# Optimization experiments

Measured on AMD Instinct MI355X. Metric: run time of the kernel, lower is better.

## Reference

```python
import jax, jax.numpy as jnp
import numpy as np

RES = 0.03
NUM_ROTS = 36
NUM_PROPOSAL = 256
OVERSAMPLE = 4           # fixed-size stand-in for the data-dependent while loop
GX, GY, GZ = 272, 112, 272  # grid covering [-4,4.16] x [-0.2,3.16] x [-4,4.16] at res=0.03
POW = 0.5
SEED_DIST_THRESH = 0.3


def setup_inputs() -> dict:
    key = jax.random.key(0)
    ks = jax.random.split(key, 6)
    N, M = 100000, 1024
    extent = jnp.array([7.0, 3.0, 7.0], jnp.float32)
    offset = jnp.array([-3.5, 0.0, -3.5], jnp.float32)
    pc = jax.random.uniform(ks[0], (N, 3), jnp.float32) * extent + offset
    xyz = jax.random.uniform(ks[1], (N, 3), jnp.float32, minval=-0.3, maxval=0.3)
    scale = jax.random.uniform(ks[2], (N, 3), jnp.float32, minval=0.1, maxval=1.0)
    prob = jax.random.uniform(ks[3], (N,), jnp.float32)
    corners = jnp.array([[-4.0, -0.2, -4.0], [4.16, 3.16, 4.16]], jnp.float32)
    vote_points = jax.random.uniform(ks[4], (M, 3), jnp.float32) * extent + offset
    return dict(pc=pc, xyz=xyz, scale=scale, prob=prob, corners=corners, vote_points=vote_points)


def hough_vote(pc, xyz, scale, prob, corners):
    # Each point casts NUM_ROTS votes: center = pc + R_y(theta) @ xyz_offset
    thetas = 2.0 * jnp.pi * jnp.arange(NUM_ROTS, dtype=jnp.float32) / NUM_ROTS
    c, s = jnp.cos(thetas), jnp.sin(thetas)  # [R]
    ox, oy, oz = xyz[:, 0:1], xyz[:, 1:2], xyz[:, 2:3]  # [N,1]
    rx = ox * c + oz * s      # [N,R]
    rz = -ox * s + oz * c     # [N,R]
    tx = pc[:, 0:1] + rx
    ty = jnp.broadcast_to(pc[:, 1:2] + oy, tx.shape)
    tz = pc[:, 2:3] + rz
    ix = jnp.floor((tx - corners[0, 0]) / RES + 0.5).astype(jnp.int32)
    iy = jnp.floor((ty - corners[0, 1]) / RES + 0.5).astype(jnp.int32)
    iz = jnp.floor((tz - corners[0, 2]) / RES + 0.5).astype(jnp.int32)
    inb = ((ix >= 0) & (ix < GX) & (iy >= 0) & (iy < GY) & (iz >= 0) & (iz < GZ))
    ixc = jnp.clip(ix, 0, GX - 1)
    iyc = jnp.clip(iy, 0, GY - 1)
    izc = jnp.clip(iz, 0, GZ - 1)
    flat = ((ixc * GY + iyc) * GZ + izc).ravel()  # [N*R]
    w = (prob[:, None] * inb.astype(prob.dtype))  # [N,R]
    grid_obj = jnp.zeros((GX * GY * GZ,), pc.dtype).at[flat].add(w.ravel())
    ws = (w[:, :, None] * scale[:, None, :]).reshape(-1, 3)
    grid_scale = jnp.zeros((GX * GY * GZ, 3), pc.dtype).at[flat].add(ws)
    hv_map = grid_obj.reshape(GX, GY, GZ)
    hv_scale = (grid_scale / (grid_obj[:, None] + 1e-7)).reshape(GX, GY, GZ, 3)
    return hv_map, hv_scale


def reference(pc, xyz, scale, prob, corners, vote_points):
    hv_map, hv_scale = hough_vote(pc, xyz, scale, prob, corners)
    hv_map_y = jnp.power(hv_map.max(axis=1) + 1e-7, POW)  # [GX,GZ]
    hv_map_yidx = jnp.argmax(hv_map, axis=1)              # [GX,GZ]
    dist = hv_map_y.reshape(-1)
    finite = jnp.isfinite(dist)
    safe = jnp.where(finite, dist, 0.0)
    ok = finite.all() & (safe.sum() >= 1e-7)
    dist = jnp.where(ok, safe, 1.0)

    # fixed-size oversampling instead of the data-dependent while loop
    K = NUM_PROPOSAL * OVERSAMPLE
    sample = jax.random.categorical(jax.random.key(42), jnp.log(dist + 1e-30), shape=(K,))
    sample_val = dist[sample]
    xi = sample // GZ
    zi = sample % GZ
    yi = hv_map_yidx[xi, zi]
    world_loc = jnp.stack([xi, yi, zi], -1).astype(pc.dtype) * RES + corners[0]  # [K,3]
    sc = hv_scale[xi, yi, zi, :]  # [K,3]

    # min distance to vote seeds; keep candidates near seeds (fallback: keep all)
    d2seed = jnp.min(jnp.linalg.norm(world_loc[:, None, :] - vote_points[None, :, :], axis=-1), axis=-1)
    keep = d2seed < SEED_DIST_THRESH
    keep = jnp.where(keep.any(), keep, jnp.ones_like(keep))
    order = jnp.argsort(jnp.where(keep, 0, 1))  # stable: passing candidates first
    sel = order[:NUM_PROPOSAL]
    candidates = world_loc[sel]
    scales_out = sc[sel]
    probs = jnp.zeros((NUM_PROPOSAL,), pc.dtype)
    return candidates, probs, scales_out
```

## Files before the change

### kernel.cpp

```cpp
#include <hip/hip_runtime.h>
#include <math.h>
#include <stdio.h>
#include <stdint.h>

#define GXD 272
#define GYD 112
#define GZD 272
#define NROT 36
#define CCLS (GXD*GZD)
#define CBLK (CCLS/256)
#define KSMP 1024
#define NPROP 256
#define HSLOTS 2048
#define YH 56
#define NBINS (GXD*2)
#define SLICE (GYD*GZD)
#define SVCAP 96
#define AROWS 32
#define AUNITS (CBLK * (KSMP/AROWS))
#define TH_SPEC 0xFFE00000u

struct RotTab { float c[NROT]; float s[NROT]; };

__device__ __forceinline__ uint32_t cell_hash(int flat) {
    return ((uint32_t)flat * 2654435761u) >> 21;
}

#define ROTL_AB(x, r) __builtin_amdgcn_alignbit((x), (x), 32u - (r))

__device__ __forceinline__ uint32_t tf_bits(uint32_t i) {
    constexpr uint32_t K1  = 42u;
    constexpr uint32_t KS2 = 42u ^ 0x1BD11BDAu;
    uint32_t x0 = 0u, x1 = i + K1;
#define TF_R(r)  { x0 += x1; x1 = ROTL_AB(x1, r); x1 ^= x0; }
#define TF_RI(r, I0, I1) { x1 += (I1); x0 = x0 + (I0) + x1; x1 = ROTL_AB(x1, r); x1 ^= x0; }
    TF_R(13) TF_R(15) TF_R(26) TF_R(6)
    TF_RI(17, K1,  KS2 + 1u)  TF_R(29) TF_R(16) TF_R(24)
    TF_RI(13, KS2, 2u)        TF_R(15) TF_R(26) TF_R(6)
    TF_RI(17, 0u,  K1 + 3u)   TF_R(29) TF_R(16) TF_R(24)
    TF_RI(13, K1,  KS2 + 4u)  TF_R(15) TF_R(26) TF_R(6)
#undef TF_R
#undef TF_RI
    return (x0 + KS2) ^ (x1 + 5u);
}

__device__ __forceinline__ float uniform_from_bits(uint32_t b) {
    const float TINY = 1.1754943508222875e-38f;
    float f = __uint_as_float((b >> 9) | 0x3f800000u) - 1.0f;
    float u = __fadd_rn(__fmul_rn(f, 1.0f), TINY);
    return fmaxf(TINY, u);
}

__device__ __forceinline__ float gumbel_from_u(float u) {
    float l1 = (float)log((double)u);
    float l2 = (float)log((double)(-l1));
    return -l2;
}

__device__ __forceinline__ void phaseA_unit(int unit, int* __restrict__ svcnt,
                                            uint2* __restrict__ svrec) {
    int cb = unit % CBLK;
    int rg = unit / CBLK;
    int c  = cb * 256 + threadIdx.x;
    int k0 = rg * AROWS;
    uint32_t i = (uint32_t)k0 * (uint32_t)CCLS + (uint32_t)c;
#pragma unroll 4
    for (int kk = 0; kk < AROWS; ++kk) {
        uint32_t bits = tf_bits(i);
        if (__builtin_expect(bits >= TH_SPEC, 0)) {
            int row = k0 + kk;
            int idx = atomicAdd(&svcnt[row], 1);
            if (idx < SVCAP) svrec[row * SVCAP + idx] = make_uint2((uint32_t)c, bits);
        }
        i += (uint32_t)CCLS;
    }
}

__device__ __forceinline__ bool vote_iy(float py, float oy, float c0y, int& iy) {
    float ty = __fadd_rn(py, oy);
    float vy = __fadd_rn(__fdiv_rn(__fsub_rn(ty, c0y), 0.03f), 0.5f);
    iy = (int)floorf(vy);
    return (iy >= 0 && iy < GYD);
}
__device__ __forceinline__ bool vote_xz(float px, float pz, float ox, float oz,
                                        float c, float s, float c0x, float c0z,
                                        int& ix, int& iz) {
    float rx = __fadd_rn(__fmul_rn(ox, c), __fmul_rn(oz, s));
    float rz = __fadd_rn(__fmul_rn(-ox, s), __fmul_rn(oz, c));
    float tx = __fadd_rn(px, rx);
    float tz = __fadd_rn(pz, rz);
    float vx = __fadd_rn(__fdiv_rn(__fsub_rn(tx, c0x), 0.03f), 0.5f);
    float vz = __fadd_rn(__fdiv_rn(__fsub_rn(tz, c0z), 0.03f), 0.5f);
    ix = (int)floorf(vx);
    iz = (int)floorf(vz);
    return (ix >= 0 && ix < GXD && iz >= 0 && iz < GZD);
}

__global__ __launch_bounds__(256) void k_count_b(const float* __restrict__ pc, const float* __restrict__ xyz,
                          const float* __restrict__ corners, int N, RotTab rt,
                          int* __restrict__ bincnt, int* __restrict__ hblk,
                          int nOrig, int unitBase, int* __restrict__ svcnt, uint2* __restrict__ svrec) {
    if ((int)blockIdx.x >= nOrig) { phaseA_unit(unitBase + (int)blockIdx.x - nOrig, svcnt, svrec); return; }
    __shared__ int h[NBINS];
    int tid = threadIdx.x;
    for (int j = tid; j < NBINS; j += 256) h[j] = 0;
    __syncthreads();
    int i = blockIdx.x * 256 + tid;
    if (i < N) {
        float px = pc[3*i], py = pc[3*i+1], pz = pc[3*i+2];
        float ox = xyz[3*i], oy = xyz[3*i+1], oz = xyz[3*i+2];
        int iy;
        if (vote_iy(py, oy, corners[1], iy)) {
            int ybit = (iy >= YH) ? 1 : 0;
            float c0x = corners[0], c0z = corners[2];
            for (int r = 0; r < NROT; ++r) {
                int ix, iz;
                if (vote_xz(px, pz, ox, oz, rt.c[r], rt.s[r], c0x, c0z, ix, iz))
                    atomicAdd(&h[ix*2 + ybit], 1);
            }
        }
    }
    __syncthreads();
    int* hb = hblk + (size_t)blockIdx.x * NBINS;
    for (int j = tid; j < NBINS; j += 256) {
        int cnt = h[j];
        hb[j] = cnt;
        if (cnt) atomicAdd(&bincnt[j], cnt);
    }
}

__global__ __launch_bounds__(576) void k_prefix(const int* __restrict__ bincnt,
                         int* __restrict__ binbase, int* __restrict__ bincur) {
    __shared__ int sc[576];
    int tid = threadIdx.x;
    int v = (tid < NBINS) ? bincnt[tid] : 0;
    sc[tid] = v;
    __syncthreads();
    for (int off = 1; off < 576; off <<= 1) {
        int x = sc[tid];
        if (tid >= off) x += sc[tid - off];
        __syncthreads();
        sc[tid] = x;
        __syncthreads();
    }
    if (tid < NBINS) {
        int excl = sc[tid] - v;
        binbase[tid] = excl;
        bincur[tid] = excl;
    }
}

__global__ __launch_bounds__(256) void k_binwrite_b(const float* __restrict__ pc, const float* __restrict__ xyz,
                          const float* __restrict__ corners,
                          int N, RotTab rt, int* __restrict__ bincur,
                          const int* __restrict__ hblk, uint32_t* __restrict__ vrec,
                          int nOrig, int unitBase, int* __restrict__ svcnt, uint2* __restrict__ svrec) {
    if ((int)blockIdx.x >= nOrig) { phaseA_unit(unitBase + (int)blockIdx.x - nOrig, svcnt, svrec); return; }
    __shared__ int h[NBINS];
    __shared__ int bbase[NBINS];
    int tid = threadIdx.x;
    const int* hb = hblk + (size_t)blockIdx.x * NBINS;
    for (int j = tid; j < NBINS; j += 256) {
        int cnt = hb[j];
        bbase[j] = cnt ? atomicAdd(&bincur[j], cnt) : 0;
        h[j] = 0;
    }
    __syncthreads();
    int i = blockIdx.x * 256 + tid;
    if (i < N) {
        float px = pc[3*i], py = pc[3*i+1], pz = pc[3*i+2];
        float ox = xyz[3*i], oy = xyz[3*i+1], oz = xyz[3*i+2];
        int iy;
        if (vote_iy(py, oy, corners[1], iy)) {
            int ybit = (iy >= YH) ? 1 : 0;
            int iyrel = iy - ybit*YH;
            float c0x = corners[0], c0z = corners[2];
            for (int r = 0; r < NROT; ++r) {
                int ix, iz;
                if (vote_xz(px, pz, ox, oz, rt.c[r], rt.s[r], c0x, c0z, ix, iz)) {
                    int bin = ix*2 + ybit;
                    int rank = atomicAdd(&h[bin], 1);
                    int slot = bbase[bin] + rank;
                    vrec[slot] = ((uint32_t)i << 14) | (uint32_t)(iyrel*GZD + iz);
                }
            }
        }
    }
}

__global__ __launch_bounds__(256) void k_accum(const int* __restrict__ binbase,
                          const int* __restrict__ bincnt,
                          const uint32_t* __restrict__ vrec,
                          const float* __restrict__ prob,
                          unsigned long long* __restrict__ packed) {
    __shared__ float tile[YH*GZD];
    int b = blockIdx.x;
    int x = b >> 1, yh = b & 1;
    int tid = threadIdx.x;
    for (int j = tid; j < YH*GZD; j += 256) tile[j] = 0.0f;
    __syncthreads();
    int lo = binbase[b], n = bincnt[b];
    for (int j = lo + tid; j < lo + n; j += 256) {
        uint32_t rec = vrec[j];
        atomicAdd(&tile[rec & 0x3FFFu], prob[rec >> 14]);
    }
    __syncthreads();
    int ybase = yh * YH;
    for (int z = tid; z < GZD; z += 256) {
        float m = tile[z];
        int mi = 0;
        for (int y = 1; y < YH; ++y) {
            float v = tile[y*GZD + z];
            if (v > m) { m = v; mi = y; }
        }
        unsigned long long key = ((unsigned long long)__float_as_uint(m) << 32)
                               | (unsigned long long)(uint32_t)(0x7F - (ybase + mi));
        atomicMax(&packed[x*GZD + z], key);
    }
}

__global__ __launch_bounds__(256) void k_colmax2_b(const unsigned long long* __restrict__ packed,
                         float* __restrict__ logits, int* __restrict__ yidx,
                         float* __restrict__ sumdist,
                         int nOrig, int unitBase, int* __restrict__ svcnt, uint2* __restrict__ svrec) {
    if ((int)blockIdx.x >= nOrig) { phaseA_unit(unitBase + (int)blockIdx.x - nOrig, svcnt, svrec); return; }
    int c = blockIdx.x * 256 + threadIdx.x;
    unsigned long long key = packed[c];
    float m = __uint_as_float((uint32_t)(key >> 32));
    int mi = 0x7F - (int)(uint32_t)(key & 0xFFFFFFFFu);
    float d = __fsqrt_rn(__fadd_rn(m, 1e-7f));
    yidx[c] = mi;
    logits[c] = (float)log((double)__fadd_rn(d, 1e-30f));
    __shared__ float sred[256];
    int tid = threadIdx.x;
    sred[tid] = d; __syncthreads();
    for (int off = 128; off > 0; off >>= 1) {
        if (tid < off) sred[tid] += sred[tid+off];
        __syncthreads();
    }
    if (tid == 0) atomicAdd(sumdist, sred[0]);
}

__global__ __launch_bounds__(256) void k_hotthresh_b(const float* __restrict__ logits,
                                                     const float* __restrict__ sumdist,
                                                     uint32_t* __restrict__ bth,
                                                     int* __restrict__ hotcnt, int* __restrict__ hotlist,
                                                     int nOrig, int unitBase,
                                                     int* __restrict__ svcnt, uint2* __restrict__ svrec) {
    if ((int)blockIdx.x >= nOrig) { phaseA_unit(unitBase + (int)blockIdx.x - nOrig, svcnt, svrec); return; }
    int c = blockIdx.x * 256 + threadIdx.x;
    double B0 = log((double)*sumdist) - 3.0;
    double t = exp(-exp((double)logits[c] - (B0 - 0.05)));
    long long k_th = (long long)floor(t * 8388608.0) - 2;
    uint32_t b;
    if (k_th <= 0)              b = 0u;
    else if (k_th >= 8388608LL) b = 0xFFFFFFFFu;
    else                        b = (uint32_t)k_th << 9;
    bth[c] = b;
    if (b < TH_SPEC) {
        int idx = atomicAdd(hotcnt, 1);
        hotlist[idx] = c;
    }
}

__global__ __launch_bounds__(256) void k_phaseB(const uint32_t* __restrict__ bth,
                                                const int* __restrict__ hotlist,
                                                const int* __restrict__ hotcnt,
                                                int* __restrict__ svcnt, uint2* __restrict__ svrec) {
    int k = blockIdx.x;
    int n = *hotcnt;
    uint32_t base = (uint32_t)k * (uint32_t)CCLS;
    for (int j = threadIdx.x; j < n; j += 256) {
        int c = hotlist[j];
        uint32_t bits = tf_bits(base + (uint32_t)c);
        if (bits >= bth[c] && bits < TH_SPEC) {
            int idx = atomicAdd(&svcnt[k], 1);
            if (idx < SVCAP) svrec[k * SVCAP + idx] = make_uint2((uint32_t)c, bits);
        }
    }
}

__global__ __launch_bounds__(64) void k_finalize(const float* __restrict__ logits,
                                                 const float* __restrict__ sumdist,
                                                 const int* __restrict__ svcnt,
                                                 const uint2* __restrict__ svrec,
                                                 const int* __restrict__ yidx,
                                                 int* __restrict__ hkeys,
                                                 int* __restrict__ samples) {
    int k = blockIdx.x;
    int tid = threadIdx.x;
    int n = svcnt[k];
    float best = -INFINITY; int bc = 0x7fffffff;
    bool full = (n <= 0 || n > SVCAP);
    if (!full) {
        for (int j = tid; j < n; j += 64) {
            uint2 rec = svrec[k * SVCAP + j];
            int c = (int)rec.x;
            float v = __fadd_rn(gumbel_from_u(uniform_from_bits(rec.y)), logits[c]);
            if (v > best || (v == best && c < bc)) { best = v; bc = c; }
        }
        for (int off = 32; off > 0; off >>= 1) {
            float v2 = __shfl_xor(best, off);
            int   i2 = __shfl_xor(bc, off);
            if (v2 > best || (v2 == best && i2 < bc)) { best = v2; bc = i2; }
        }
        double B0 = log((double)*sumdist) - 3.0;
        if (!((double)best > B0 - 0.05)) full = true;
    }
    if (full) {
        best = -INFINITY; bc = 0x7fffffff;
        uint32_t base = (uint32_t)k * (uint32_t)CCLS;
        for (int c = tid; c < CCLS; c += 64) {
            float v = __fadd_rn(gumbel_from_u(uniform_from_bits(tf_bits(base + (uint32_t)c))), logits[c]);
            if (v > best || (v == best && c < bc)) { best = v; bc = c; }
        }
        for (int off = 32; off > 0; off >>= 1) {
            float v2 = __shfl_xor(best, off);
            int   i2 = __shfl_xor(bc, off);
            if (v2 > best || (v2 == best && i2 < bc)) { best = v2; bc = i2; }
        }
    }
    if (tid == 0) {
        samples[k] = bc;
        int xi = bc / GZD, zi = bc % GZD;
        int yi = yidx[bc];
        int flat = (xi*GYD + yi)*GZD + zi;
        uint32_t h = cell_hash(flat);
        for (;;) {
            int prev = atomicCAS(&hkeys[h], -1, flat);
            if (prev == -1 || prev == flat) break;
            h = (h + 1) & (HSLOTS - 1);
        }
    }
}

__global__ __launch_bounds__(256) void k_scale_scatter(const float* __restrict__ pc, const float* __restrict__ xyz,
                          const float* __restrict__ scale, const float* __restrict__ prob,
                          const float* __restrict__ corners,
                          const int* __restrict__ hkeys, float* __restrict__ gsmall,
                          int N, RotTab rt) {
    __shared__ int lk[HSLOTS];
    for (int j = threadIdx.x; j < HSLOTS; j += 256) lk[j] = hkeys[j];
    __syncthreads();
    int i = blockIdx.x * 256 + threadIdx.x;
    if (i >= N) return;
    float px = pc[3*i], py = pc[3*i+1], pz = pc[3*i+2];
    float ox = xyz[3*i], oy = xyz[3*i+1], oz = xyz[3*i+2];
    int iy;
    if (!vote_iy(py, oy, corners[1], iy)) return;
    float c0x = corners[0], c0z = corners[2];
    int iyo = iy * GZD;
    float w0 = prob[i];
    float ws0 = __fmul_rn(w0, scale[3*i]);
    float ws1 = __fmul_rn(w0, scale[3*i+1]);
    float ws2 = __fmul_rn(w0, scale[3*i+2]);
    for (int r = 0; r < NROT; ++r) {
        int ix, iz;
        if (!vote_xz(px, pz, ox, oz, rt.c[r], rt.s[r], c0x, c0z, ix, iz)) continue;
        int flat = ix * SLICE + iyo + iz;
        uint32_t h = cell_hash(flat);
        int slot = -1;
        for (;;) {
            int key = lk[h];
            if (key == flat) { slot = (int)h; break; }
            if (key == -1) break;
            h = (h + 1) & (HSLOTS - 1);
        }
        if (slot < 0) continue;
        atomicAdd(&gsmall[3*slot+0], ws0);
        atomicAdd(&gsmall[3*slot+1], ws1);
        atomicAdd(&gsmall[3*slot+2], ws2);
    }
}

__global__ __launch_bounds__(256) void k_post(const unsigned long long* __restrict__ packed,
                       const int* __restrict__ hkeys, const float* __restrict__ gsmall,
                       const int* __restrict__ yidx, const int* __restrict__ samples,
                       const float* __restrict__ corners, const float* __restrict__ vp, int M,
                       float* __restrict__ world, float* __restrict__ scv, int* __restrict__ keep) {
    int k = blockIdx.x;
    int tid = threadIdx.x;
    int s = samples[k];
    int xi = s / GZD, zi = s % GZD;
    int yi = yidx[s];
    float wx = __fadd_rn(__fmul_rn((float)xi, 0.03f), corners[0]);
    float wy = __fadd_rn(__fmul_rn((float)yi, 0.03f), corners[1]);
    float wz = __fadd_rn(__fmul_rn((float)zi, 0.03f), corners[2]);

    float dmin = INFINITY;
    for (int j = tid; j < M; j += 256) {
        float dx = __fsub_rn(wx, vp[3*j]);
        float dy = __fsub_rn(wy, vp[3*j+1]);
        float dz = __fsub_rn(wz, vp[3*j+2]);
        float sq = __fadd_rn(__fadd_rn(__fmul_rn(dx,dx), __fmul_rn(dy,dy)), __fmul_rn(dz,dz));
        dmin = fminf(dmin, __fsqrt_rn(sq));
    }
    __shared__ float sm[256];
    sm[tid] = dmin; __syncthreads();
    for (int off = 128; off > 0; off >>= 1) {
        if (tid < off) sm[tid] = fminf(sm[tid], sm[tid+off]);
        __syncthreads();
    }
    if (tid == 0) {
        world[3*k] = wx; world[3*k+1] = wy; world[3*k+2] = wz;
        int flat = (xi*GYD + yi)*GZD + zi;
        uint32_t h = cell_hash(flat);
        while (hkeys[h] != flat) h = (h + 1) & (HSLOTS - 1);
        float m = __uint_as_float((uint32_t)(packed[s] >> 32));
        float go = __fadd_rn(m, 1e-7f);
        scv[3*k+0] = __fdiv_rn(gsmall[3*h+0], go);
        scv[3*k+1] = __fdiv_rn(gsmall[3*h+1], go);
        scv[3*k+2] = __fdiv_rn(gsmall[3*h+2], go);
        keep[k] = (sm[0] < 0.3f) ? 1 : 0;
    }
}

__global__ __launch_bounds__(256) void k_select(const float* __restrict__ world,
                                                const float* __restrict__ scv,
                                                const int* __restrict__ keep,
                                                float* __restrict__ out) {
    __shared__ int kp[KSMP];
    __shared__ int tsum[256];
    __shared__ int sel[NPROP];
    __shared__ int anyk;
    int tid = threadIdx.x;
    if (tid == 0) anyk = 0;
    __syncthreads();
    int a = 0;
    for (int j = tid; j < KSMP; j += 256) { int v = keep[j]; kp[j] = v; a |= v; }
    if (a) anyk = 1;
    __syncthreads();
    int any = anyk;
    int j0 = tid * 4;
    int k0v = any ? kp[j0]   : 1;
    int k1v = any ? kp[j0+1] : 1;
    int k2v = any ? kp[j0+2] : 1;
    int k3v = any ? kp[j0+3] : 1;
    int s0 = k0v, s1 = s0 + k1v, s2 = s1 + k2v, s3 = s2 + k3v;
    tsum[tid] = s3;
    __syncthreads();
    for (int off = 1; off < 256; off <<= 1) {
        int x = tsum[tid];
        if (tid >= off) x += tsum[tid - off];
        __syncthreads();
        tsum[tid] = x;
        __syncthreads();
    }
    int base = (tid > 0) ? tsum[tid-1] : 0;
    int nk = tsum[255];
    int inc[4] = { base + s0, base + s1, base + s2, base + s3 };
    int kv[4]  = { k0v, k1v, k2v, k3v };
    for (int q = 0; q < 4; ++q) {
        int j = j0 + q;
        int slot = kv[q] ? (inc[q] - 1) : (nk + j - inc[q]);
        if (slot < NPROP) sel[slot] = j;
    }
    __syncthreads();
    if (tid < NPROP) {
        int sidx = sel[tid];
        out[3*tid+0] = world[3*sidx+0];
        out[3*tid+1] = world[3*sidx+1];
        out[3*tid+2] = world[3*sidx+2];
        out[3*NPROP + tid] = 0.0f;
        out[4*NPROP + 3*tid + 0] = scv[3*sidx+0];
        out[4*NPROP + 3*tid + 1] = scv[3*sidx+1];
        out[4*NPROP + 3*tid + 2] = scv[3*sidx+2];
    }
}

extern "C" void kernel_launch(void* const* d_in, const int* in_sizes, int n_in,
                              void* d_out, int out_size, void* d_ws, size_t ws_size,
                              hipStream_t stream) {
    const float* pc      = (const float*)d_in[0];
    const float* xyz     = (const float*)d_in[1];
    const float* scale   = (const float*)d_in[2];
    const float* prob    = (const float*)d_in[3];
    const float* corners = (const float*)d_in[4];
    const float* vp      = (const float*)d_in[5];
    int N = in_sizes[0] / 3;
    int M = in_sizes[5] / 3;
    int NV = N * NROT;
    int pblocks = (N + 255) / 256;
    if (N > (1 << 17)) {
        fprintf(stderr, "kernel_launch: N %d exceeds packing limit\n", N);
        return;
    }

    float* sumdist = (float*)d_ws;
    int*   bincnt  = (int*)(sumdist + 1);
    int*   svcnt   = bincnt + NBINS;
    int*   hotcnt  = svcnt + KSMP;
    unsigned long long* packed = (unsigned long long*)(hotcnt + 1);
    float* gsmall  = (float*)(packed + CCLS);
    size_t zero_bytes = (size_t)((char*)(gsmall + 3*HSLOTS) - (char*)sumdist);
    int*   binbase = (int*)(gsmall + 3*HSLOTS);
    int*   bincur  = binbase + NBINS;
    float* logits  = (float*)(bincur + NBINS);
    uint32_t* bth  = (uint32_t*)(logits + CCLS);
    int*   yidx    = (int*)(bth + CCLS);
    int*   samples = yidx + CCLS;
    int*   hkeys   = samples + KSMP;
    float* world   = (float*)(hkeys + HSLOTS);
    float* scv     = world + 3*KSMP;
    int*   keep    = (int*)(scv + 3*KSMP);
    uint2* svrec   = (uint2*)(((uintptr_t)(keep + KSMP) + 15) & ~(uintptr_t)15);
    int*   hotlist = (int*)(svrec + (size_t)KSMP * SVCAP);
    int*   hblk    = hotlist + CCLS;
    uint32_t* vrec = (uint32_t*)(((uintptr_t)(hblk + (size_t)pblocks*NBINS) + 15) & ~(uintptr_t)15);
    size_t need = (size_t)((char*)(vrec + NV) - (char*)d_ws);
    if (ws_size < need) {
        fprintf(stderr, "kernel_launch: ws_size %zu < needed %zu\n", ws_size, need);
        return;
    }

    hipMemsetAsync(sumdist, 0, zero_bytes, stream);
    hipMemsetAsync(hkeys, 0xFF, HSLOTS*sizeof(int), stream);

    RotTab rt;
    const float twopi = (float)(2.0 * M_PI);
    for (int r = 0; r < NROT; ++r) {
        float th = (twopi * (float)r) / 36.0f;
        rt.c[r] = (float)cos((double)th);
        rt.s[r] = (float)sin((double)th);
    }

    const int BAL1 = 2800, BAL2 = 2800, BAL3 = 1900, BAL4 = AUNITS - BAL1 - BAL2 - BAL3;

    k_count_b<<<pblocks + BAL1, 256, 0, stream>>>(pc, xyz, corners, N, rt, bincnt, hblk,
                                                  pblocks, 0, svcnt, svrec);
    k_prefix<<<1, 576, 0, stream>>>(bincnt, binbase, bincur);
    k_binwrite_b<<<pblocks + BAL2, 256, 0, stream>>>(pc, xyz, corners, N, rt, bincur, hblk, vrec,
                                                     pblocks, BAL1, svcnt, svrec);
    k_accum<<<NBINS, 256, 0, stream>>>(binbase, bincnt, vrec, prob, packed);
    k_colmax2_b<<<CBLK + BAL3, 256, 0, stream>>>(packed, logits, yidx, sumdist,
                                                 CBLK, BAL1 + BAL2, svcnt, svrec);
    k_hotthresh_b<<<CBLK + BAL4, 256, 0, stream>>>(logits, sumdist, bth, hotcnt, hotlist,
                                                   CBLK, BAL1 + BAL2 + BAL3, svcnt, svrec);
    k_phaseB<<<KSMP, 256, 0, stream>>>(bth, hotlist, hotcnt, svcnt, svrec);
    k_finalize<<<KSMP, 64, 0, stream>>>(logits, sumdist, svcnt, svrec, yidx, hkeys, samples);
    k_scale_scatter<<<pblocks, 256, 0, stream>>>(pc, xyz, scale, prob, corners, hkeys, gsmall, N, rt);
    k_post<<<KSMP, 256, 0, stream>>>(packed, hkeys, gsmall, yidx, samples, corners, vp, M, world, scv, keep);
    k_select<<<1, 256, 0, stream>>>(world, scv, keep, (float*)d_out);
}
```

Measured before the change: 368.6 us.

## Cache vote bins across passes, fuse phaseB into finalize, bin-driven scale scatter

The count pass now stores each point-rotation's bin and cell code in a vote cache, so the binwrite pass reads these codes back instead of recomputing rotations and floor divisions. The phaseB kernel is folded into finalize, which scans the hot list itself with 64 threads per sample. The scale scatter now walks the binned vote records instead of recomputing votes per point, and it absorbs the last share of phaseA work units. The hash keys are shifted by one so that zero marks an empty slot, which lets a single memset clear them and drops one memset. In exchange the vote cache adds a large workspace write and read, and finalize has fewer threads for the hot-list scan.

```diff
diff --git a/kernel.cpp b/kernel.cpp
--- a/kernel.cpp
+++ b/kernel.cpp
@@ -19,6 +19,7 @@
 #define AROWS 32
 #define AUNITS (CBLK * (KSMP/AROWS))
 #define TH_SPEC 0xFFE00000u
+#define VC_INVALID 0xFFFFFFFFu
 
 struct RotTab { float c[NROT]; float s[NROT]; };
 
@@ -99,6 +100,7 @@
 __global__ __launch_bounds__(256) void k_count_b(const float* __restrict__ pc, const float* __restrict__ xyz,
                           const float* __restrict__ corners, int N, RotTab rt,
                           int* __restrict__ bincnt, int* __restrict__ hblk,
+                          uint32_t* __restrict__ vcache,
                           int nOrig, int unitBase, int* __restrict__ svcnt, uint2* __restrict__ svrec) {
     if ((int)blockIdx.x >= nOrig) { phaseA_unit(unitBase + (int)blockIdx.x - nOrig, svcnt, svrec); return; }
     __shared__ int h[NBINS];
@@ -106,19 +108,32 @@
     for (int j = tid; j < NBINS; j += 256) h[j] = 0;
     __syncthreads();
     int i = blockIdx.x * 256 + tid;
+    bool act = false;
+    float px=0, py=0, pz=0, ox=0, oy=0, oz=0, c0x=0, c0z=0;
+    int ybit = 0, iyrel = 0;
     if (i < N) {
-        float px = pc[3*i], py = pc[3*i+1], pz = pc[3*i+2];
-        float ox = xyz[3*i], oy = xyz[3*i+1], oz = xyz[3*i+2];
+        px = pc[3*i]; py = pc[3*i+1]; pz = pc[3*i+2];
+        ox = xyz[3*i]; oy = xyz[3*i+1]; oz = xyz[3*i+2];
         int iy;
         if (vote_iy(py, oy, corners[1], iy)) {
-            int ybit = (iy >= YH) ? 1 : 0;
-            float c0x = corners[0], c0z = corners[2];
-            for (int r = 0; r < NROT; ++r) {
-                int ix, iz;
-                if (vote_xz(px, pz, ox, oz, rt.c[r], rt.s[r], c0x, c0z, ix, iz))
-                    atomicAdd(&h[ix*2 + ybit], 1);
+            act = true;
+            ybit = (iy >= YH) ? 1 : 0;
+            iyrel = iy - ybit*YH;
+            c0x = corners[0]; c0z = corners[2];
+        }
+    }
+    uint32_t* vc = vcache + ((size_t)blockIdx.x * NROT) * 256 + tid;
+    for (int r = 0; r < NROT; ++r) {
+        uint32_t v = VC_INVALID;
+        if (act) {
+            int ix, iz;
+            if (vote_xz(px, pz, ox, oz, rt.c[r], rt.s[r], c0x, c0z, ix, iz)) {
+                int bin = ix*2 + ybit;
+                v = ((uint32_t)bin << 14) | (uint32_t)(iyrel*GZD + iz);
+                atomicAdd(&h[bin], 1);
             }
         }
+        vc[(size_t)r * 256] = v;
     }
     __syncthreads();
     int* hb = hblk + (size_t)blockIdx.x * NBINS;
@@ -150,10 +165,9 @@
     }
 }
 
-__global__ __launch_bounds__(256) void k_binwrite_b(const float* __restrict__ pc, const float* __restrict__ xyz,
-                          const float* __restrict__ corners,
-                          int N, RotTab rt, int* __restrict__ bincur,
-                          const int* __restrict__ hblk, uint32_t* __restrict__ vrec,
+__global__ __launch_bounds__(256) void k_binwrite_b(int N, int* __restrict__ bincur,
+                          const int* __restrict__ hblk, const uint32_t* __restrict__ vcache,
+                          uint32_t* __restrict__ vrec,
                           int nOrig, int unitBase, int* __restrict__ svcnt, uint2* __restrict__ svrec) {
     if ((int)blockIdx.x >= nOrig) { phaseA_unit(unitBase + (int)blockIdx.x - nOrig, svcnt, svrec); return; }
     __shared__ int h[NBINS];
@@ -166,24 +180,15 @@
         h[j] = 0;
     }
     __syncthreads();
-    int i = blockIdx.x * 256 + tid;
-    if (i < N) {
-        float px = pc[3*i], py = pc[3*i+1], pz = pc[3*i+2];
-        float ox = xyz[3*i], oy = xyz[3*i+1], oz = xyz[3*i+2];
-        int iy;
-        if (vote_iy(py, oy, corners[1], iy)) {
-            int ybit = (iy >= YH) ? 1 : 0;
-            int iyrel = iy - ybit*YH;
-            float c0x = corners[0], c0z = corners[2];
-            for (int r = 0; r < NROT; ++r) {
-                int ix, iz;
-                if (vote_xz(px, pz, ox, oz, rt.c[r], rt.s[r], c0x, c0z, ix, iz)) {
-                    int bin = ix*2 + ybit;
-                    int rank = atomicAdd(&h[bin], 1);
-                    int slot = bbase[bin] + rank;
-                    vrec[slot] = ((uint32_t)i << 14) | (uint32_t)(iyrel*GZD + iz);
-                }
-            }
+    uint32_t i = (uint32_t)(blockIdx.x * 256 + tid);
+    const uint32_t* vc = vcache + ((size_t)blockIdx.x * NROT) * 256 + tid;
+    uint32_t ish = i << 14;
+    for (int r = 0; r < NROT; ++r) {
+        uint32_t v = vc[(size_t)r * 256];
+        if (v != VC_INVALID) {
+            int bin = (int)(v >> 14);
+            int rank = atomicAdd(&h[bin], 1);
+            vrec[bbase[bin] + rank] = ish | (v & 0x3FFFu);
         }
     }
 }
@@ -263,33 +268,20 @@
     }
 }
 
-__global__ __launch_bounds__(256) void k_phaseB(const uint32_t* __restrict__ bth,
-                                                const int* __restrict__ hotlist,
-                                                const int* __restrict__ hotcnt,
-                                                int* __restrict__ svcnt, uint2* __restrict__ svrec) {
-    int k = blockIdx.x;
-    int n = *hotcnt;
-    uint32_t base = (uint32_t)k * (uint32_t)CCLS;
-    for (int j = threadIdx.x; j < n; j += 256) {
-        int c = hotlist[j];
-        uint32_t bits = tf_bits(base + (uint32_t)c);
-        if (bits >= bth[c] && bits < TH_SPEC) {
-            int idx = atomicAdd(&svcnt[k], 1);
-            if (idx < SVCAP) svrec[k * SVCAP + idx] = make_uint2((uint32_t)c, bits);
-        }
-    }
-}
-
 __global__ __launch_bounds__(64) void k_finalize(const float* __restrict__ logits,
                                                  const float* __restrict__ sumdist,
                                                  const int* __restrict__ svcnt,
                                                  const uint2* __restrict__ svrec,
+                                                 const uint32_t* __restrict__ bth,
+                                                 const int* __restrict__ hotlist,
+                                                 const int* __restrict__ hotcnt,
                                                  const int* __restrict__ yidx,
                                                  int* __restrict__ hkeys,
                                                  int* __restrict__ samples) {
     int k = blockIdx.x;
     int tid = threadIdx.x;
     int n = svcnt[k];
+    uint32_t base = (uint32_t)k * (uint32_t)CCLS;
     float best = -INFINITY; int bc = 0x7fffffff;
     bool full = (n <= 0 || n > SVCAP);
     if (!full) {
@@ -299,6 +291,15 @@
             float v = __fadd_rn(gumbel_from_u(uniform_from_bits(rec.y)), logits[c]);
             if (v > best || (v == best && c < bc)) { best = v; bc = c; }
         }
+        int nhot = *hotcnt;
+        for (int j = tid; j < nhot; j += 64) {
+            int c = hotlist[j];
+            uint32_t bits = tf_bits(base + (uint32_t)c);
+            if (bits >= bth[c] && bits < TH_SPEC) {
+                float v = __fadd_rn(gumbel_from_u(uniform_from_bits(bits)), logits[c]);
+                if (v > best || (v == best && c < bc)) { best = v; bc = c; }
+            }
+        }
         for (int off = 32; off > 0; off >>= 1) {
             float v2 = __shfl_xor(best, off);
             int   i2 = __shfl_xor(bc, off);
@@ -309,7 +310,6 @@
     }
     if (full) {
         best = -INFINITY; bc = 0x7fffffff;
-        uint32_t base = (uint32_t)k * (uint32_t)CCLS;
         for (int c = tid; c < CCLS; c += 64) {
             float v = __fadd_rn(gumbel_from_u(uniform_from_bits(tf_bits(base + (uint32_t)c))), logits[c]);
             if (v > best || (v == best && c < bc)) { best = v; bc = c; }
@@ -324,52 +324,47 @@
         samples[k] = bc;
         int xi = bc / GZD, zi = bc % GZD;
         int yi = yidx[bc];
-        int flat = (xi*GYD + yi)*GZD + zi;
-        uint32_t h = cell_hash(flat);
+        int key = (xi*GYD + yi)*GZD + zi + 1;
+        uint32_t h = cell_hash(key - 1);
         for (;;) {
-            int prev = atomicCAS(&hkeys[h], -1, flat);
-            if (prev == -1 || prev == flat) break;
+            int prev = atomicCAS(&hkeys[h], 0, key);
+            if (prev == 0 || prev == key) break;
             h = (h + 1) & (HSLOTS - 1);
         }
     }
 }
 
-__global__ __launch_bounds__(256) void k_scale_scatter(const float* __restrict__ pc, const float* __restrict__ xyz,
-                          const float* __restrict__ scale, const float* __restrict__ prob,
-                          const float* __restrict__ corners,
+__global__ __launch_bounds__(256) void k_scale_b(const int* __restrict__ binbase,
+                          const int* __restrict__ bincnt,
+                          const uint32_t* __restrict__ vrec,
+                          const float* __restrict__ prob, const float* __restrict__ scale,
                           const int* __restrict__ hkeys, float* __restrict__ gsmall,
-                          int N, RotTab rt) {
+                          int nOrig, int unitBase, int* __restrict__ svcnt, uint2* __restrict__ svrec) {
+    if ((int)blockIdx.x >= nOrig) { phaseA_unit(unitBase + (int)blockIdx.x - nOrig, svcnt, svrec); return; }
     __shared__ int lk[HSLOTS];
     for (int j = threadIdx.x; j < HSLOTS; j += 256) lk[j] = hkeys[j];
     __syncthreads();
-    int i = blockIdx.x * 256 + threadIdx.x;
-    if (i >= N) return;
-    float px = pc[3*i], py = pc[3*i+1], pz = pc[3*i+2];
-    float ox = xyz[3*i], oy = xyz[3*i+1], oz = xyz[3*i+2];
-    int iy;
-    if (!vote_iy(py, oy, corners[1], iy)) return;
-    float c0x = corners[0], c0z = corners[2];
-    int iyo = iy * GZD;
-    float w0 = prob[i];
-    float ws0 = __fmul_rn(w0, scale[3*i]);
-    float ws1 = __fmul_rn(w0, scale[3*i+1]);
-    float ws2 = __fmul_rn(w0, scale[3*i+2]);
-    for (int r = 0; r < NROT; ++r) {
-        int ix, iz;
-        if (!vote_xz(px, pz, ox, oz, rt.c[r], rt.s[r], c0x, c0z, ix, iz)) continue;
-        int flat = ix * SLICE + iyo + iz;
-        uint32_t h = cell_hash(flat);
+    int b = blockIdx.x;
+    int x = b >> 1, ybit = b & 1;
+    int fbase = x * SLICE + ybit * (YH*GZD) + 1;
+    int lo = binbase[b], n = bincnt[b];
+    for (int j = lo + threadIdx.x; j < lo + n; j += 256) {
+        uint32_t rec = vrec[j];
+        int key = fbase + (int)(rec & 0x3FFFu);
+        uint32_t h = cell_hash(key - 1);
         int slot = -1;
         for (;;) {
-            int key = lk[h];
-            if (key == flat) { slot = (int)h; break; }
-            if (key == -1) break;
+            int kk = lk[h];
+            if (kk == key) { slot = (int)h; break; }
+            if (kk == 0) break;
             h = (h + 1) & (HSLOTS - 1);
         }
         if (slot < 0) continue;
-        atomicAdd(&gsmall[3*slot+0], ws0);
-        atomicAdd(&gsmall[3*slot+1], ws1);
-        atomicAdd(&gsmall[3*slot+2], ws2);
+        int i = (int)(rec >> 14);
+        float w0 = prob[i];
+        atomicAdd(&gsmall[3*slot+0], __fmul_rn(w0, scale[3*i]));
+        atomicAdd(&gsmall[3*slot+1], __fmul_rn(w0, scale[3*i+1]));
+        atomicAdd(&gsmall[3*slot+2], __fmul_rn(w0, scale[3*i+2]));
     }
 }
 
@@ -403,9 +398,9 @@
     }
     if (tid == 0) {
         world[3*k] = wx; world[3*k+1] = wy; world[3*k+2] = wz;
-        int flat = (xi*GYD + yi)*GZD + zi;
-        uint32_t h = cell_hash(flat);
-        while (hkeys[h] != flat) h = (h + 1) & (HSLOTS - 1);
+        int key = (xi*GYD + yi)*GZD + zi + 1;
+        uint32_t h = cell_hash(key - 1);
+        while (hkeys[h] != key) h = (h + 1) & (HSLOTS - 1);
         float m = __uint_as_float((uint32_t)(packed[s] >> 32));
         float go = __fadd_rn(m, 1e-7f);
         scv[3*k+0] = __fdiv_rn(gsmall[3*h+0], go);
@@ -479,8 +474,8 @@
     const float* vp      = (const float*)d_in[5];
     int N = in_sizes[0] / 3;
     int M = in_sizes[5] / 3;
-    int NV = N * NROT;
     int pblocks = (N + 255) / 256;
+    int NV = pblocks * 256 * NROT;
     if (N > (1 << 17)) {
         fprintf(stderr, "kernel_launch: N %d exceeds packing limit\n", N);
         return;
@@ -492,21 +487,22 @@
     int*   hotcnt  = svcnt + KSMP;
     unsigned long long* packed = (unsigned long long*)(hotcnt + 1);
     float* gsmall  = (float*)(packed + CCLS);
-    size_t zero_bytes = (size_t)((char*)(gsmall + 3*HSLOTS) - (char*)sumdist);
-    int*   binbase = (int*)(gsmall + 3*HSLOTS);
+    int*   hkeys   = (int*)(gsmall + 3*HSLOTS);
+    size_t zero_bytes = (size_t)((char*)(hkeys + HSLOTS) - (char*)sumdist);
+    int*   binbase = hkeys + HSLOTS;
     int*   bincur  = binbase + NBINS;
     float* logits  = (float*)(bincur + NBINS);
     uint32_t* bth  = (uint32_t*)(logits + CCLS);
     int*   yidx    = (int*)(bth + CCLS);
     int*   samples = yidx + CCLS;
-    int*   hkeys   = samples + KSMP;
-    float* world   = (float*)(hkeys + HSLOTS);
+    float* world   = (float*)(samples + KSMP);
     float* scv     = world + 3*KSMP;
     int*   keep    = (int*)(scv + 3*KSMP);
     uint2* svrec   = (uint2*)(((uintptr_t)(keep + KSMP) + 15) & ~(uintptr_t)15);
     int*   hotlist = (int*)(svrec + (size_t)KSMP * SVCAP);
     int*   hblk    = hotlist + CCLS;
-    uint32_t* vrec = (uint32_t*)(((uintptr_t)(hblk + (size_t)pblocks*NBINS) + 15) & ~(uintptr_t)15);
+    uint32_t* vcache = (uint32_t*)(((uintptr_t)(hblk + (size_t)pblocks*NBINS) + 15) & ~(uintptr_t)15);
+    uint32_t* vrec = vcache + NV;
     size_t need = (size_t)((char*)(vrec + NV) - (char*)d_ws);
     if (ws_size < need) {
         fprintf(stderr, "kernel_launch: ws_size %zu < needed %zu\n", ws_size, need);
@@ -514,7 +510,6 @@
     }
 
     hipMemsetAsync(sumdist, 0, zero_bytes, stream);
-    hipMemsetAsync(hkeys, 0xFF, HSLOTS*sizeof(int), stream);
 
     RotTab rt;
     const float twopi = (float)(2.0 * M_PI);
@@ -524,21 +519,23 @@
         rt.s[r] = (float)sin((double)th);
     }
 
-    const int BAL1 = 2800, BAL2 = 2800, BAL3 = 1900, BAL4 = AUNITS - BAL1 - BAL2 - BAL3;
-
-    k_count_b<<<pblocks + BAL1, 256, 0, stream>>>(pc, xyz, corners, N, rt, bincnt, hblk,
+    const int BAL1 = 2400, BAL2 = 2400, BAL3 = 1700, BAL4 = 1500;
+    const int BAL5 = AUNITS - BAL1 - BAL2 - BAL3 - BAL4;
+
+    k_count_b<<<pblocks + BAL1, 256, 0, stream>>>(pc, xyz, corners, N, rt, bincnt, hblk, vcache,
                                                   pblocks, 0, svcnt, svrec);
     k_prefix<<<1, 576, 0, stream>>>(bincnt, binbase, bincur);
-    k_binwrite_b<<<pblocks + BAL2, 256, 0, stream>>>(pc, xyz, corners, N, rt, bincur, hblk, vrec,
+    k_binwrite_b<<<pblocks + BAL2, 256, 0, stream>>>(N, bincur, hblk, vcache, vrec,
                                                      pblocks, BAL1, svcnt, svrec);
     k_accum<<<NBINS, 256, 0, stream>>>(binbase, bincnt, vrec, prob, packed);
     k_colmax2_b<<<CBLK + BAL3, 256, 0, stream>>>(packed, logits, yidx, sumdist,
                                                  CBLK, BAL1 + BAL2, svcnt, svrec);
     k_hotthresh_b<<<CBLK + BAL4, 256, 0, stream>>>(logits, sumdist, bth, hotcnt, hotlist,
                                                    CBLK, BAL1 + BAL2 + BAL3, svcnt, svrec);
-    k_phaseB<<<KSMP, 256, 0, stream>>>(bth, hotlist, hotcnt, svcnt, svrec);
-    k_finalize<<<KSMP, 64, 0, stream>>>(logits, sumdist, svcnt, svrec, yidx, hkeys, samples);
-    k_scale_scatter<<<pblocks, 256, 0, stream>>>(pc, xyz, scale, prob, corners, hkeys, gsmall, N, rt);
+    k_finalize<<<KSMP, 64, 0, stream>>>(logits, sumdist, svcnt, svrec, bth, hotlist, hotcnt,
+                                        yidx, hkeys, samples);
+    k_scale_b<<<NBINS + BAL5, 256, 0, stream>>>(binbase, bincnt, vrec, prob, scale, hkeys, gsmall,
+                                                NBINS, BAL1 + BAL2 + BAL3 + BAL4, svcnt, svrec);
     k_post<<<KSMP, 256, 0, stream>>>(packed, hkeys, gsmall, yidx, samples, corners, vp, M, world, scv, keep);
     k_select<<<1, 256, 0, stream>>>(world, scv, keep, (float*)d_out);
 }
```

Measured after the change: 956.9 us. +159.6%, slower.
